# Kernel optimization log

Hardware: AMD Instinct MI355X
Metric: run time of the kernel (lower is better)

## Reference

```python
import jax, jax.numpy as jnp
import numpy as np

NUM_LATENT = 1024
LATENT_DIM = 256
BETA = 0.25
N_TOKENS = 65536


def setup_inputs() -> dict:
    key = jax.random.key(0)
    k1, k2 = jax.random.split(key)
    latent_embedding = jax.random.normal(k1, (N_TOKENS, LATENT_DIM), dtype=jnp.float32)
    # torch.nn.init.uniform_(codebook, -1/num_latent, 1/num_latent)
    codebook = jax.random.uniform(
        k2, (NUM_LATENT, LATENT_DIM), dtype=jnp.float32,
        minval=-1.0 / NUM_LATENT, maxval=1.0 / NUM_LATENT)
    return {"latent_embedding": latent_embedding, "codebook": codebook}


def reference(latent_embedding, codebook):
    le_det = jax.lax.stop_gradient(latent_embedding)  # [N, D]
    # distances[n,k] = ||z_n||^2 + ||c_k||^2 - 2 z_n . c_k   (z detached, codebook NOT)
    distances = (jnp.sum(le_det ** 2, axis=1, keepdims=True)
                 + jnp.sum(codebook ** 2, axis=1)
                 - 2.0 * jnp.matmul(le_det, codebook.T))  # [N, K]
    encoding_inds = jnp.argmin(distances, axis=1)  # [N]
    # one_hot @ codebook == gather rows of codebook
    quantized_latents = codebook[encoding_inds]  # [N, D]
    num_latent = codebook.shape[0]
    commitment_loss = jnp.mean((jax.lax.stop_gradient(quantized_latents)
                                - latent_embedding) ** 2) * num_latent
    embedding_loss = jnp.mean((quantized_latents - le_det) ** 2) * num_latent
    vq_loss = embedding_loss + commitment_loss * BETA
    probs = jax.nn.softmax(-distances, axis=1)  # [N, K]
    probs = jnp.clip(jnp.mean(probs, axis=0, keepdims=True), 0.001, 0.999)  # [1, K]
    return (quantized_latents, codebook, probs, vq_loss)
```

## Files before the change

kernel.cpp:

```cpp
#include <hip/hip_runtime.h>

#define N_TOK 65536
#define DIM   256
#define K_CODES 1024
#define CB_OFF    16777216
#define PROBS_OFF (16777216 + 262144)
#define LOSS_OFF  (16777216 + 262144 + 1024)
#define TM 64

typedef float  f32x4  __attribute__((ext_vector_type(4)));
typedef short  s16x8  __attribute__((ext_vector_type(8)));

__device__ __forceinline__ unsigned short f32_to_bf16(float x) {
    unsigned u = __float_as_uint(x);
    unsigned r = (u + 0x7FFFu + ((u >> 16) & 1u)) >> 16;
    return (unsigned short)r;
}
__device__ __forceinline__ unsigned fkey(float a) {
    unsigned u = __float_as_uint(a);
    unsigned m = (unsigned)(((int)u) >> 31);
    return u ^ (m | 0x80000000u);
}
__device__ __forceinline__ float fkey_inv(unsigned k) {
    unsigned u = (k & 0x80000000u) ? (k ^ 0x80000000u) : ~k;
    return __uint_as_float(u);
}

__global__ __launch_bounds__(512) void k_prep(const float* __restrict__ cb,
                                              float* __restrict__ c2,
                                              unsigned short* __restrict__ cbf,
                                              float* __restrict__ probs_part,
                                              float* __restrict__ lossR,
                                              float* __restrict__ outcb,
                                              int zcount, int nloss, int docopy) {
    const int g  = blockIdx.x;
    const int t  = threadIdx.x;
    const int wv = t >> 6;
    const int ln = t & 63;
    const int l15 = ln & 15, q = ln >> 4;

    const float* zp = cb + (size_t)(g * 16 + l15) * DIM + wv * 32 + q * 8;
    f32x4 z0 = *(const f32x4*)(zp);
    f32x4 z1 = *(const f32x4*)(zp + 4);
    s16x8 a;
    a[0] = (short)f32_to_bf16(z0[0]); a[1] = (short)f32_to_bf16(z0[1]);
    a[2] = (short)f32_to_bf16(z0[2]); a[3] = (short)f32_to_bf16(z0[3]);
    a[4] = (short)f32_to_bf16(z1[0]); a[5] = (short)f32_to_bf16(z1[1]);
    a[6] = (short)f32_to_bf16(z1[2]); a[7] = (short)f32_to_bf16(z1[3]);
    *(s16x8*)(cbf + (size_t)(g * 8 + wv) * 1024 + ln * 8) = a;

    float s = z0[0]*z0[0] + z0[1]*z0[1] + z0[2]*z0[2] + z0[3]*z0[3]
            + z1[0]*z1[0] + z1[1]*z1[1] + z1[2]*z1[2] + z1[3]*z1[3];
    s += __shfl_xor(s, 16, 64);
    s += __shfl_xor(s, 32, 64);
    __shared__ float c2p[8][16];
    if (q == 0) c2p[wv][l15] = s;

    const int base = g * 512 + t;
    if (base < nloss) lossR[base] = 0.f;
    if (base < zcount) probs_part[base] = 0.f;
    if (base + 32768 < zcount) probs_part[base + 32768] = 0.f;
    if (docopy) {
        #pragma unroll
        for (int i = 0; i < 8; i++) outcb[base + i * 32768] = cb[base + i * 32768];
    }

    __syncthreads();
    if (t < 16) {
        float acc = 0.f;
        #pragma unroll
        for (int ww = 0; ww < 8; ww++) acc += c2p[ww][t];
        c2[g * 16 + t] = acc;
    }
}

__global__ __launch_bounds__(1024, 4) void k_main(const float* __restrict__ z,
                                                  const float* __restrict__ cb,
                                                  const unsigned short* __restrict__ cbf,
                                                  const float* __restrict__ c2,
                                                  float* __restrict__ out_q,
                                                  float* __restrict__ probs_part,
                                                  float* __restrict__ lossR,
                                                  int repmask) {
    const int t   = threadIdx.x;
    const int w   = t >> 6;
    const int ln  = t & 63;
    const int q   = ln >> 4;
    const int l15 = ln & 15;
    const int k0  = w * 64;
    const int n0  = blockIdx.x * TM;
    float* pp = probs_part + (blockIdx.x & repmask) * K_CODES;

    __shared__ unsigned short a_lds[32 * 64 * 8];
    __shared__ float    z2p[32][16];
    __shared__ unsigned kred[16][64];
    __shared__ float    ered[16][64];
    __shared__ int   fidx[64];
    __shared__ float fU[64];

    #pragma unroll
    for (int rep = 0; rep < 2; rep++) {
        const int f   = t + rep * 1024;
        const int md  = w + rep * 16;
        const int m   = md >> 3;
        const int dsv = md & 7;
        const int row = m * 16 + l15;
        const int dim = dsv * 32 + q * 8;
        const float* zp = z + (size_t)(n0 + row) * DIM + dim;
        f32x4 z0 = *(const f32x4*)(zp);
        f32x4 z1 = *(const f32x4*)(zp + 4);
        s16x8 a;
        a[0] = (short)f32_to_bf16(z0[0]); a[1] = (short)f32_to_bf16(z0[1]);
        a[2] = (short)f32_to_bf16(z0[2]); a[3] = (short)f32_to_bf16(z0[3]);
        a[4] = (short)f32_to_bf16(z1[0]); a[5] = (short)f32_to_bf16(z1[1]);
        a[6] = (short)f32_to_bf16(z1[2]); a[7] = (short)f32_to_bf16(z1[3]);
        *(s16x8*)(a_lds + (size_t)f * 8) = a;
        float s = z0[0]*z0[0] + z0[1]*z0[1] + z0[2]*z0[2] + z0[3]*z0[3]
                + z1[0]*z1[0] + z1[1]*z1[1] + z1[2]*z1[2] + z1[3]*z1[3];
        s += __shfl_xor(s, 16, 64);
        s += __shfl_xor(s, 32, 64);
        if (q == 0) z2p[md][l15] = s;
    }

    float c2v[4];
    #pragma unroll
    for (int nt = 0; nt < 4; nt++) c2v[nt] = c2[k0 + nt * 16 + l15];
    f32x4 acc[4][4];
    #pragma unroll
    for (int m = 0; m < 4; m++)
        #pragma unroll
        for (int nt = 0; nt < 4; nt++) {
            const float iv = -0.5f * c2v[nt];
            f32x4 v4 = {iv, iv, iv, iv};
            acc[m][nt] = v4;
        }

    __syncthreads();

    const unsigned short* bb = cbf + (size_t)(w * 4) * 8 * 1024 + ln * 8;
    #pragma unroll
    for (int ds = 0; ds < 8; ds++) {
        s16x8 af[4];
        #pragma unroll
        for (int m = 0; m < 4; m++)
            af[m] = *(const s16x8*)(a_lds + (size_t)((m * 8 + ds) * 64 + ln) * 8);
        #pragma unroll
        for (int nt = 0; nt < 4; nt++) {
            s16x8 b = *(const s16x8*)(bb + (size_t)(nt * 8 + ds) * 1024);
            #pragma unroll
            for (int m = 0; m < 4; m++)
                acc[m][nt] = __builtin_amdgcn_mfma_f32_16x16x32_bf16(af[m], b, acc[m][nt], 0, 0, 0);
        }
    }

    unsigned lkey[4][4];
    float    lesum[4][4];
    #pragma unroll
    for (int m = 0; m < 4; m++)
        #pragma unroll
        for (int v = 0; v < 4; v++) { lkey[m][v] = 0u; lesum[m][v] = 0.f; }

    #pragma unroll
    for (int m = 0; m < 4; m++)
        #pragma unroll
        for (int nt = 0; nt < 4; nt++) {
            const unsigned colc = 1023u - (unsigned)(k0 + nt * 16 + l15);
            #pragma unroll
            for (int v = 0; v < 4; v++) {
                float a = acc[m][nt][v];
                unsigned key = (fkey(a) & 0xFFFFFC00u) | colc;
                lkey[m][v] = max(lkey[m][v], key);
                float e = __expf(a + a);
                acc[m][nt][v] = e;
                lesum[m][v] += e;
            }
        }

    #pragma unroll
    for (int off = 1; off < 16; off <<= 1) {
        #pragma unroll
        for (int m = 0; m < 4; m++)
            #pragma unroll
            for (int v = 0; v < 4; v++) {
                unsigned ok = (unsigned)__shfl_xor((int)lkey[m][v], off, 64);
                float    oe = __shfl_xor(lesum[m][v], off, 64);
                lkey[m][v] = max(lkey[m][v], ok);
                lesum[m][v] += oe;
            }
    }

    if (l15 == 0) {
        #pragma unroll
        for (int m = 0; m < 4; m++)
            #pragma unroll
            for (int v = 0; v < 4; v++) {
                const int r = m * 16 + q * 4 + v;
                kred[w][r] = lkey[m][v]; ered[w][r] = lesum[m][v];
            }
    }
    __syncthreads();
    float lossreg = 0.f;
    if (t < 64) {
        unsigned bk = kred[0][t];
        float U = ered[0][t];
        #pragma unroll
        for (int ww = 1; ww < 16; ww++) {
            bk = max(bk, kred[ww][t]);
            U += ered[ww][t];
        }
        fidx[t] = 1023 - (int)(bk & 1023u);
        fU[t] = U;
        float a_rec = fkey_inv(bk);
        float z2 = 0.f;
        #pragma unroll
        for (int ds = 0; ds < 8; ds++) z2 += z2p[(t >> 4) * 8 + ds][t & 15];
        lossreg = z2 - 2.0f * a_rec;
    }
    __syncthreads();

    float ps[4];
    #pragma unroll
    for (int nt = 0; nt < 4; nt++) ps[nt] = 0.f;
    #pragma unroll
    for (int m = 0; m < 4; m++)
        #pragma unroll
        for (int v = 0; v < 4; v++) {
            const float invU = 1.0f / fU[m * 16 + q * 4 + v];
            #pragma unroll
            for (int nt = 0; nt < 4; nt++) ps[nt] += acc[m][nt][v] * invU;
        }
    #pragma unroll
    for (int nt = 0; nt < 4; nt++) {
        ps[nt] += __shfl_xor(ps[nt], 16, 64);
        ps[nt] += __shfl_xor(ps[nt], 32, 64);
    }
    atomicAdd(&pp[k0 + q * 16 + l15], ps[q]);

    #pragma unroll
    for (int i = 0; i < 4; i++) {
        const int r  = w * 4 + i;
        const int am = fidx[r];
        f32x4 qv = *(const f32x4*)(cb + (size_t)am * DIM + ln * 4);
        *(f32x4*)(out_q + (size_t)(n0 + r) * DIM + ln * 4) = qv;
    }

    if (w == 0) {
        #pragma unroll
        for (int off = 32; off; off >>= 1) lossreg += __shfl_down(lossreg, off, 64);
        if (ln == 0) atomicAdd(&lossR[blockIdx.x & 63], lossreg);
    }
}

__global__ __launch_bounds__(256) void k_fin(const float* __restrict__ cb,
                                             const float* __restrict__ probs_part,
                                             const float* __restrict__ lossR,
                                             float* __restrict__ out,
                                             int R, int nLoss, int docopy) {
    const int g = blockIdx.x * 256 + threadIdx.x;
    if (docopy && g < 262144) out[CB_OFF + g] = cb[g];
    if (g < K_CODES) {
        float a0 = 0.f, a1 = 0.f, a2 = 0.f, a3 = 0.f;
        if (R >= 4) {
            for (int r = 0; r < R; r += 4) {
                a0 += probs_part[(r + 0) * K_CODES + g];
                a1 += probs_part[(r + 1) * K_CODES + g];
                a2 += probs_part[(r + 2) * K_CODES + g];
                a3 += probs_part[(r + 3) * K_CODES + g];
            }
        } else {
            for (int r = 0; r < R; r++) a0 += probs_part[r * K_CODES + g];
        }
        float p = (a0 + a1 + a2 + a3) * (1.0f / 65536.0f);
        p = fminf(fmaxf(p, 0.001f), 0.999f);
        out[PROBS_OFF + g] = p;
    }
    if (g == 0) {
        float ls = 0.f;
        for (int r = 0; r < nLoss; r++) ls += lossR[r];
        out[LOSS_OFF] = ls * (1280.0f / 16777216.0f);
    }
}

extern "C" void kernel_launch(void* const* d_in, const int* in_sizes, int n_in,
                              void* d_out, int out_size, void* d_ws, size_t ws_size,
                              hipStream_t stream) {
    (void)in_sizes; (void)n_in; (void)out_size;
    const float* z  = (const float*)d_in[0];
    const float* cb = (const float*)d_in[1];
    float* out = (float*)d_out;

    float* c2 = (float*)d_ws;

    float *probs_part, *lossR;
    int R, nLoss;
    size_t used = 1024 * 4;
    auto fits = [&](int r) { return ws_size >= used + (size_t)(64 + r * 1024) * 4; };
    if      (fits(64)) R = 64;
    else if (fits(16)) R = 16;
    else if (fits(4))  R = 4;
    else               R = 0;
    if (R) {
        lossR      = c2 + 1024;
        probs_part = lossR + 64;
        nLoss = 64;
        used += (size_t)(64 + R * 1024) * 4;
    } else {
        probs_part = out + PROBS_OFF;
        lossR      = out + LOSS_OFF;
        R = 1; nLoss = 1;
    }

    unsigned short* cbf;
    int cbf_in_ws = (ws_size >= used + (size_t)K_CODES * DIM * 2);
    if (cbf_in_ws) cbf = (unsigned short*)((char*)d_ws + used);
    else           cbf = (unsigned short*)(out + CB_OFF);

    k_prep<<<dim3(64), dim3(512), 0, stream>>>(cb, c2, cbf, probs_part, lossR,
                                               out + CB_OFF, R * 1024, nLoss, cbf_in_ws);
    k_main<<<dim3(N_TOK / TM), dim3(1024), 0, stream>>>(z, cb, cbf, c2, out, probs_part,
                                                        lossR, R - 1);
    const int fin_blocks = cbf_in_ws ? 4 : 1024;
    k_fin<<<dim3(fin_blocks), dim3(256), 0, stream>>>(cb, probs_part, lossR, out,
                                                      R, nLoss, !cbf_in_ws);
}
```

Measured before the change: 209.7 us.

## Store per-block softmax partials instead of atomics and use DPP row reductions

When the workspace is large enough, each k_main block writes its column-probability partial sums to its own row, with no atomicAdd. This removes atomic contention and the zeroing pass in k_prep. k_fin then reduces the 1024 rows with 16 blocks, splitting the rows into four chunks per column and combining them through shared memory. Separately, the 16-lane max/sum reductions over argmin keys and exp-sums now use DPP row-permute intrinsics instead of shfl_xor. The trade-off is a 4 MB partials buffer that must be written and read back, plus a serial final reduction.

```diff
diff --git a/kernel.cpp b/kernel.cpp
--- a/kernel.cpp
+++ b/kernel.cpp
@@ -24,6 +24,23 @@
 __device__ __forceinline__ float fkey_inv(unsigned k) {
     unsigned u = (k & 0x80000000u) ? (k ^ 0x80000000u) : ~k;
     return __uint_as_float(u);
+}
+
+__device__ __forceinline__ unsigned red16_max_u(unsigned v) {
+    unsigned t;
+    t = (unsigned)__builtin_amdgcn_update_dpp(0, (int)v, 0xB1,  0xF, 0xF, true); v = v > t ? v : t;
+    t = (unsigned)__builtin_amdgcn_update_dpp(0, (int)v, 0x4E,  0xF, 0xF, true); v = v > t ? v : t;
+    t = (unsigned)__builtin_amdgcn_update_dpp(0, (int)v, 0x141, 0xF, 0xF, true); v = v > t ? v : t;
+    t = (unsigned)__builtin_amdgcn_update_dpp(0, (int)v, 0x140, 0xF, 0xF, true); v = v > t ? v : t;
+    return v;
+}
+__device__ __forceinline__ float red16_sum_f(float v) {
+    float t;
+    t = __uint_as_float((unsigned)__builtin_amdgcn_update_dpp(0, (int)__float_as_uint(v), 0xB1,  0xF, 0xF, true)); v += t;
+    t = __uint_as_float((unsigned)__builtin_amdgcn_update_dpp(0, (int)__float_as_uint(v), 0x4E,  0xF, 0xF, true)); v += t;
+    t = __uint_as_float((unsigned)__builtin_amdgcn_update_dpp(0, (int)__float_as_uint(v), 0x141, 0xF, 0xF, true)); v += t;
+    t = __uint_as_float((unsigned)__builtin_amdgcn_update_dpp(0, (int)__float_as_uint(v), 0x140, 0xF, 0xF, true)); v += t;
+    return v;
 }
 
 __global__ __launch_bounds__(512) void k_prep(const float* __restrict__ cb,
@@ -89,7 +106,8 @@
     const int l15 = ln & 15;
     const int k0  = w * 64;
     const int n0  = blockIdx.x * TM;
-    float* pp = probs_part + (blockIdx.x & repmask) * K_CODES;
+    float* pp = probs_part +
+        (size_t)((repmask < 0) ? (int)blockIdx.x : (int)(blockIdx.x & repmask)) * K_CODES;
 
     __shared__ unsigned short a_lds[32 * 64 * 8];
     __shared__ float    z2p[32][16];
@@ -177,17 +195,12 @@
         }
 
     #pragma unroll
-    for (int off = 1; off < 16; off <<= 1) {
-        #pragma unroll
-        for (int m = 0; m < 4; m++)
-            #pragma unroll
-            for (int v = 0; v < 4; v++) {
-                unsigned ok = (unsigned)__shfl_xor((int)lkey[m][v], off, 64);
-                float    oe = __shfl_xor(lesum[m][v], off, 64);
-                lkey[m][v] = max(lkey[m][v], ok);
-                lesum[m][v] += oe;
-            }
-    }
+    for (int m = 0; m < 4; m++)
+        #pragma unroll
+        for (int v = 0; v < 4; v++) {
+            lkey[m][v]  = red16_max_u(lkey[m][v]);
+            lesum[m][v] = red16_sum_f(lesum[m][v]);
+        }
 
     if (l15 == 0) {
         #pragma unroll
@@ -234,7 +247,8 @@
         ps[nt] += __shfl_xor(ps[nt], 16, 64);
         ps[nt] += __shfl_xor(ps[nt], 32, 64);
     }
-    atomicAdd(&pp[k0 + q * 16 + l15], ps[q]);
+    if (repmask < 0) pp[k0 + q * 16 + l15] = ps[q];
+    else             atomicAdd(&pp[k0 + q * 16 + l15], ps[q]);
 
     #pragma unroll
     for (int i = 0; i < 4; i++) {
@@ -257,8 +271,30 @@
                                              float* __restrict__ out,
                                              int R, int nLoss, int docopy) {
     const int g = blockIdx.x * 256 + threadIdx.x;
+    __shared__ float part[4][64];
     if (docopy && g < 262144) out[CB_OFF + g] = cb[g];
-    if (g < K_CODES) {
+    if (R == 1024) {
+        if (blockIdx.x < 16) {
+            const int col   = blockIdx.x * 64 + (threadIdx.x & 63);
+            const int chunk = threadIdx.x >> 6;
+            const float* p0 = probs_part + (size_t)chunk * 256 * K_CODES + col;
+            float a0 = 0.f, a1 = 0.f, a2 = 0.f, a3 = 0.f;
+            for (int r = 0; r < 256; r += 4) {
+                a0 += p0[(size_t)(r + 0) * K_CODES];
+                a1 += p0[(size_t)(r + 1) * K_CODES];
+                a2 += p0[(size_t)(r + 2) * K_CODES];
+                a3 += p0[(size_t)(r + 3) * K_CODES];
+            }
+            part[chunk][threadIdx.x & 63] = a0 + a1 + a2 + a3;
+            __syncthreads();
+            if (threadIdx.x < 64) {
+                float p = (part[0][threadIdx.x] + part[1][threadIdx.x]
+                         + part[2][threadIdx.x] + part[3][threadIdx.x]) * (1.0f / 65536.0f);
+                p = fminf(fmaxf(p, 0.001f), 0.999f);
+                out[PROBS_OFF + blockIdx.x * 64 + threadIdx.x] = p;
+            }
+        }
+    } else if (g < K_CODES) {
         float a0 = 0.f, a1 = 0.f, a2 = 0.f, a3 = 0.f;
         if (R >= 4) {
             for (int r = 0; r < R; r += 4) {
@@ -292,22 +328,25 @@
     float* c2 = (float*)d_ws;
 
     float *probs_part, *lossR;
-    int R, nLoss;
+    int R, nLoss, repmask;
     size_t used = 1024 * 4;
     auto fits = [&](int r) { return ws_size >= used + (size_t)(64 + r * 1024) * 4; };
-    if      (fits(64)) R = 64;
-    else if (fits(16)) R = 16;
-    else if (fits(4))  R = 4;
-    else               R = 0;
+    if      (fits(1024)) R = 1024;
+    else if (fits(64))   R = 64;
+    else if (fits(16))   R = 16;
+    else if (fits(4))    R = 4;
+    else                 R = 0;
+    const int storeMode = (R == 1024);
     if (R) {
         lossR      = c2 + 1024;
         probs_part = lossR + 64;
         nLoss = 64;
         used += (size_t)(64 + R * 1024) * 4;
+        repmask = storeMode ? -1 : (R - 1);
     } else {
         probs_part = out + PROBS_OFF;
         lossR      = out + LOSS_OFF;
-        R = 1; nLoss = 1;
+        R = 1; nLoss = 1; repmask = 0;
     }
 
     unsigned short* cbf;
@@ -316,10 +355,11 @@
     else           cbf = (unsigned short*)(out + CB_OFF);
 
     k_prep<<<dim3(64), dim3(512), 0, stream>>>(cb, c2, cbf, probs_part, lossR,
-                                               out + CB_OFF, R * 1024, nLoss, cbf_in_ws);
+                                               out + CB_OFF, storeMode ? 0 : R * 1024,
+                                               nLoss, cbf_in_ws);
     k_main<<<dim3(N_TOK / TM), dim3(1024), 0, stream>>>(z, cb, cbf, c2, out, probs_part,
-                                                        lossR, R - 1);
-    const int fin_blocks = cbf_in_ws ? 4 : 1024;
+                                                        lossR, repmask);
+    const int fin_blocks = cbf_in_ws ? (storeMode ? 16 : 4) : 1024;
     k_fin<<<dim3(fin_blocks), dim3(256), 0, stream>>>(cb, probs_part, lossR, out,
                                                       R, nLoss, !cbf_in_ws);
 }
```

Result: slower. 217.5 us (+3.7%).
